# Optimization experiments

Hardware: AMD Instinct MI355X
Metric: run time of the kernel (lower is better)

Reference implementation:

```python
import jax, jax.numpy as jnp
import numpy as np

N = 50000      # nodes
E = 800000     # edges
D_IN = 128
D_H = 128
D_OUT = 64
P = 0.3        # dropout prob


def _glorot(key, out_c, in_c):
    return jax.random.normal(key, (out_c, in_c), jnp.float32) * (1.0 / np.sqrt(in_c))


def setup_inputs() -> dict:
    key = jax.random.key(0)
    ks = jax.random.split(key, 10)
    return {
        "x": jax.random.normal(ks[0], (N, D_IN), jnp.float32),
        "u1": jax.random.uniform(ks[1], (N, D_H), jnp.float32),
        "u2": jax.random.uniform(ks[2], (N, D_H), jnp.float32),
        "wl0": _glorot(ks[3], D_H, D_IN), "bl0": jnp.zeros((D_H,), jnp.float32), "wr0": _glorot(ks[4], D_H, D_IN),
        "wl1": _glorot(ks[5], D_H, D_H), "bl1": jnp.zeros((D_H,), jnp.float32), "wr1": _glorot(ks[6], D_H, D_H),
        "wl2": _glorot(ks[7], D_OUT, D_H), "bl2": jnp.zeros((D_OUT,), jnp.float32), "wr2": _glorot(ks[8], D_OUT, D_H),
        "edge_index": jax.random.randint(ks[9], (2, E), 0, N),
    }


def _sage_conv(x, src, dst, wl, bl, wr):
    # PyG SAGEConv (aggr='mean'): lin_l(mean of neighbor msgs) + lin_r(x)
    msg = x[src]                                                    # [E, d] gather
    s = jax.ops.segment_sum(msg, dst, num_segments=N)               # [N, d] scatter-sum
    cnt = jax.ops.segment_sum(jnp.ones((dst.shape[0],), x.dtype), dst, num_segments=N)
    mean = s / jnp.maximum(cnt, 1.0)[:, None]                       # mean; 0 for isolated nodes
    return mean @ wl.T + bl + x @ wr.T


def reference(x, u1, u2, wl0, bl0, wr0, wl1, bl1, wr1, wl2, bl2, wr2, edge_index):
    src, dst = edge_index[0], edge_index[1]
    keep = 1.0 - P
    h = jax.nn.relu(_sage_conv(x, src, dst, wl0, bl0, wr0))
    h = h * ((u1 >= P).astype(h.dtype) / keep)                      # dropout (training=True)
    h = jax.nn.relu(_sage_conv(h, src, dst, wl1, bl1, wr1))
    h = h * ((u2 >= P).astype(h.dtype) / keep)
    return _sage_conv(h, src, dst, wl2, bl2, wr2)
```

## Files before the change

### kernel.cpp

```cpp
#include <hip/hip_runtime.h>


constexpr int N = 50000;
constexpr int E = 800000;
constexpr int NBUCK = (N + 255) / 256;
constexpr int CE = 4096;
constexpr int NEB = (E + CE - 1) / CE;
constexpr int SLOT = 6208;
static_assert(N <= 65536, "u16 packing");
static_assert(N % 16 == 0, "16-row blocks need no bounds checks");

typedef _Float16 f16x8 __attribute__((ext_vector_type(8)));
typedef _Float16 f16x4 __attribute__((ext_vector_type(4)));
typedef _Float16 f16x2 __attribute__((ext_vector_type(2)));
typedef float f32x4 __attribute__((ext_vector_type(4)));
typedef unsigned short u16x8 __attribute__((ext_vector_type(8)));
typedef unsigned short u16x4 __attribute__((ext_vector_type(4)));

constexpr int CONVB = (N * 128 / 8 + 255) / 256;
constexpr int MASKB = (N * 128) / (8 * 256);

__device__ inline void wfrag_build(int idx, int KB, const float* wl,
                                   const float* wr, _Float16* wf) {
  int j = idx & 7;
  int lane = (idx >> 3) & 63;
  int kb = (idx >> 9) % KB;
  int ct = (idx >> 9) / KB;
  int c = ct * 16 + (lane & 15);
  int k = kb * 32 + (lane >> 4) * 8 + j;
  float v = (k < 128) ? wl[c * 128 + k] : wr[c * 128 + (k - 128)];
  wf[idx] = (_Float16)v;
}

__global__ __launch_bounds__(256) void setup_scatter_kernel(
    const int* __restrict__ src, const int* __restrict__ dst,
    int* __restrict__ bcur, unsigned* __restrict__ T,
    const float* __restrict__ x,
    const float* __restrict__ u1, const float* __restrict__ u2,
    const float* __restrict__ wl0, const float* __restrict__ wr0,
    const float* __restrict__ wl1, const float* __restrict__ wr1,
    const float* __restrict__ wl2, const float* __restrict__ wr2,
    _Float16* __restrict__ HA, _Float16* __restrict__ wf0,
    _Float16* __restrict__ wf1, _Float16* __restrict__ wfZ,
    unsigned* __restrict__ mk1, unsigned* __restrict__ mk2) {
  __shared__ unsigned sorted[CE];
  __shared__ int hist[256], scan[256], excl[256], lcur[256], gbase[256];
  const int b = blockIdx.x;
  const int t = threadIdx.x;
  if (b < NEB) {
    const int e0 = b * CE;
    const int nval = min(CE, E - e0);
    hist[t] = 0;
    __syncthreads();
    for (int i = t; i < nval; i += 256) atomicAdd(&hist[dst[e0 + i] >> 8], 1);
    __syncthreads();
    const int h = hist[t];
    scan[t] = h;
    __syncthreads();
    for (int off = 1; off < 256; off <<= 1) {
      int u = (t >= off) ? scan[t - off] : 0;
      __syncthreads();
      scan[t] += u;
      __syncthreads();
    }
    excl[t] = scan[t] - h;
    lcur[t] = scan[t] - h;
    gbase[t] = (t < NBUCK && h > 0) ? (t * SLOT + atomicAdd(&bcur[t], h)) : 0;
    __syncthreads();
    for (int i = t; i < nval; i += 256) {
      int e = e0 + i;
      int d = dst[e];
      int p = atomicAdd(&lcur[d >> 8], 1);
      sorted[p] = ((unsigned)d << 16) | (unsigned)src[e];
    }
    __syncthreads();
    for (int i = t; i < nval; i += 256) {
      unsigned pk = sorted[i];
      int bb = pk >> 24;
      T[gbase[bb] + (i - excl[bb])] = pk;
    }
    return;
  }
  const int b2 = b - NEB;
  if (b2 < CONVB) {
    int i = b2 * 256 + t;
    if (i < N * 128 / 8) {
      float4 a = ((const float4*)x)[i * 2];
      float4 c = ((const float4*)x)[i * 2 + 1];
      f16x8 v;
      v[0] = (_Float16)a.x; v[1] = (_Float16)a.y; v[2] = (_Float16)a.z; v[3] = (_Float16)a.w;
      v[4] = (_Float16)c.x; v[5] = (_Float16)c.y; v[6] = (_Float16)c.z; v[7] = (_Float16)c.w;
      ((f16x8*)HA)[i] = v;
    }
  } else if (b2 < CONVB + 128) {
    wfrag_build((b2 - CONVB) * 256 + t, 8, wl0, wr0, wf0);
  } else if (b2 < CONVB + 256) {
    wfrag_build((b2 - CONVB - 128) * 256 + t, 8, wl1, wr1, wf1);
  } else if (b2 < CONVB + 320) {
    int idx = (b2 - CONVB - 256) * 256 + t;
    int j = idx & 7;
    int lane = (idx >> 3) & 63;
    int kb = (idx >> 9) & 3;
    int ct = idx >> 11;
    int c = ct * 16 + (lane & 15);
    int k = kb * 32 + (lane >> 4) * 8 + j;
    float v = (c < 64) ? wl2[c * 128 + k] : wr2[(c - 64) * 128 + k];
    wfZ[idx] = (_Float16)v;
  } else {
    int mb = b2 - (CONVB + 320);
    const float* Us = (mb < MASKB) ? u1 : u2;
    unsigned* MKs = (mb < MASKB) ? mk1 : mk2;
    int bb = (mb < MASKB) ? mb : (mb - MASKB);
#pragma unroll
    for (int k = 0; k < 8; ++k) {
      int i = (bb * 8 + k) * 256 + t;
      unsigned long long m = __ballot(Us[i] >= 0.3f);
      int lt = t & 63;
      if (lt == 0) MKs[i >> 5] = (unsigned)m;
      else if (lt == 32) MKs[i >> 5] = (unsigned)(m >> 32);
    }
  }
}

__global__ __launch_bounds__(256) void bucket_place_kernel(
    const unsigned* __restrict__ T, const int* __restrict__ bcur,
    int* __restrict__ offs, int* __restrict__ deg,
    unsigned short* __restrict__ elist) {
  __shared__ int dcnt[256], s[256], ncur[256];
  const int t = threadIdx.x;
  const int b = blockIdx.x;
  const int lo = b * SLOT;
  const int hi = lo + bcur[b];
  dcnt[t] = 0;
  __syncthreads();
  for (int i = lo + t; i < hi; i += 256) atomicAdd(&dcnt[(T[i] >> 16) & 255], 1);
  __syncthreads();
  const int v = dcnt[t];
  const int pv = (v + 7) & ~7;
  s[t] = pv;
  __syncthreads();
  for (int off = 1; off < 256; off <<= 1) {
    int u = (t >= off) ? s[t - off] : 0;
    __syncthreads();
    s[t] += u;
    __syncthreads();
  }
  const int base = lo + s[t] - pv;
  const int node = b * 256 + t;
  if (node < N) { offs[node] = base; deg[node] = v; }
  ncur[t] = base;
  __syncthreads();
  for (int i = lo + t; i < hi; i += 256) {
    unsigned pk = T[i];
    int pos = atomicAdd(&ncur[(pk >> 16) & 255], 1);
    elist[pos] = (unsigned short)(pk & 0xffffu);
  }
}

__device__ __forceinline__ void gather_mean_wide(
    const _Float16* __restrict__ H, const unsigned short* __restrict__ elist,
    int e0, int d, int g, int cl, float* acc ) {
  const int e1 = e0 + d;
  int e = e0;
  for (; e + 16 <= e1; e += 16) {
    u16x8 q0 = *(const u16x8*)(elist + e);
    u16x8 q1 = *(const u16x8*)(elist + e + 8);
    int s[16] = {q0[0], q0[1], q0[2], q0[3], q0[4], q0[5], q0[6], q0[7],
                 q1[0], q1[1], q1[2], q1[3], q1[4], q1[5], q1[6], q1[7]};
    f16x8 v[8];
#pragma unroll
    for (int u = 0; u < 8; ++u)
      v[u] = *(const f16x8*)(H + (size_t)s[2 * u + g] * 128 + cl * 8);
#pragma unroll
    for (int u = 0; u < 8; ++u)
#pragma unroll
      for (int j = 0; j < 8; ++j) acc[j] += (float)v[u][j];
  }
  for (; e + 2 <= e1; e += 2) {
    int s0 = elist[e + g];
    f16x8 v = *(const f16x8*)(H + (size_t)s0 * 128 + cl * 8);
#pragma unroll
    for (int j = 0; j < 8; ++j) acc[j] += (float)v[j];
  }
  if (e < e1 && g == 0) {
    f16x8 v = *(const f16x8*)(H + (size_t)elist[e] * 128 + cl * 8);
#pragma unroll
    for (int j = 0; j < 8; ++j) acc[j] += (float)v[j];
  }
#pragma unroll
  for (int j = 0; j < 8; ++j) acc[j] += __shfl_xor(acc[j], 16);
}

__global__ __launch_bounds__(256, 6) void fused_layer_kernel(
    const _Float16* __restrict__ H, const int* __restrict__ offs,
    const int* __restrict__ deg, const unsigned short* __restrict__ elist,
    const _Float16* __restrict__ Wf, const float* __restrict__ bias,
    const unsigned* __restrict__ MK, _Float16* __restrict__ outp) {
  __shared__ __align__(16) _Float16 Af[8][64][8];
  const int t = threadIdx.x;
  const int rowbase = blockIdx.x * 16;

  {
    int r = t >> 4, o = t & 15;
    f16x8 v = *(const f16x8*)(H + (size_t)(rowbase + r) * 128 + o * 8);
    *(f16x8*)&Af[4 + (o >> 2)][(o & 3) * 16 + r][0] = v;
  }

  {
    const int hw = t >> 5;
    const int ll = t & 31;
    const int g = ll >> 4;
    const int cl = ll & 15;
#pragma unroll 1
    for (int i = 0; i < 2; ++i) {
      int r = hw * 2 + i;
      int node = rowbase + r;
      float acc[8] = {0.f, 0.f, 0.f, 0.f, 0.f, 0.f, 0.f, 0.f};
      const int d = deg[node];
      gather_mean_wide(H, elist, offs[node], d, g, cl, acc);
      if (g == 0) {
        float inv = 1.0f / (float)max(d, 1);
        f16x8 o;
#pragma unroll
        for (int j = 0; j < 8; ++j) o[j] = (_Float16)(acc[j] * inv);
        *(f16x8*)&Af[cl >> 2][(cl & 3) * 16 + r][0] = o;
      }
    }
  }
  __syncthreads();

  const int lane = t & 63;
  const int w = t >> 6;
  const int n16 = lane & 15;
  const int qq = lane >> 4;
  const int colbase = w * 32;

  f32x4 acc[2];
  acc[0] = (f32x4){0.f, 0.f, 0.f, 0.f};
  acc[1] = (f32x4){0.f, 0.f, 0.f, 0.f};

#pragma unroll
  for (int kb = 0; kb < 8; ++kb) {
    f16x8 a = *(const f16x8*)&Af[kb][lane][0];
#pragma unroll
    for (int ct = 0; ct < 2; ++ct) {
      const int ctg = w * 2 + ct;
      f16x8 b = *(const f16x8*)(Wf + ((size_t)(ctg * 8 + kb) * 64 + lane) * 8);
      acc[ct] = __builtin_amdgcn_mfma_f32_16x16x32_f16(a, b, acc[ct], 0, 0, 0);
    }
  }

#pragma unroll
  for (int r = 0; r < 4; ++r) {
    int row = rowbase + qq * 4 + r;
    unsigned mw = MK[(size_t)row * 4 + w];
#pragma unroll
    for (int ct = 0; ct < 2; ++ct) {
      const int col = colbase + ct * 16 + n16;
      float v = fmaxf(acc[ct][r] + bias[col], 0.f);
      v = ((mw >> (ct * 16 + n16)) & 1u) ? v * (1.0f / 0.7f) : 0.0f;
      outp[(size_t)row * 128 + col] = (_Float16)v;
    }
  }
}

__global__ __launch_bounds__(256, 6) void fused_layerZ_kernel(
    const _Float16* __restrict__ H, const int* __restrict__ offs,
    const int* __restrict__ deg, const unsigned short* __restrict__ elist,
    const _Float16* __restrict__ Wf, const float* __restrict__ bias,
    const unsigned* __restrict__ MK, const _Float16* __restrict__ WfZ,
    const float* __restrict__ bl2, _Float16* __restrict__ Y2,
    float* __restrict__ F) {
  __shared__ __align__(16) _Float16 Af[8][64][8];
  __shared__ __align__(16) _Float16 Zf[16][136];
  const int t = threadIdx.x;
  const int rowbase = blockIdx.x * 16;

  {
    int r = t >> 4, o = t & 15;
    f16x8 v = *(const f16x8*)(H + (size_t)(rowbase + r) * 128 + o * 8);
    *(f16x8*)&Af[4 + (o >> 2)][(o & 3) * 16 + r][0] = v;
  }

  {
    const int hw = t >> 5;
    const int ll = t & 31;
    const int g = ll >> 4;
    const int cl = ll & 15;
#pragma unroll 1
    for (int i = 0; i < 2; ++i) {
      int r = hw * 2 + i;
      int node = rowbase + r;
      float acc[8] = {0.f, 0.f, 0.f, 0.f, 0.f, 0.f, 0.f, 0.f};
      const int d = deg[node];
      gather_mean_wide(H, elist, offs[node], d, g, cl, acc);
      if (g == 0) {
        float inv = 1.0f / (float)max(d, 1);
        f16x8 o;
#pragma unroll
        for (int j = 0; j < 8; ++j) o[j] = (_Float16)(acc[j] * inv);
        *(f16x8*)&Af[cl >> 2][(cl & 3) * 16 + r][0] = o;
      }
    }
  }
  __syncthreads();

  const int lane = t & 63;
  const int w = t >> 6;
  const int n16 = lane & 15;
  const int qq = lane >> 4;
  const int colbase = w * 32;

  f32x4 acc[2];
  acc[0] = (f32x4){0.f, 0.f, 0.f, 0.f};
  acc[1] = (f32x4){0.f, 0.f, 0.f, 0.f};

#pragma unroll
  for (int kb = 0; kb < 8; ++kb) {
    f16x8 a = *(const f16x8*)&Af[kb][lane][0];
#pragma unroll
    for (int ct = 0; ct < 2; ++ct) {
      const int ctg = w * 2 + ct;
      f16x8 b = *(const f16x8*)(Wf + ((size_t)(ctg * 8 + kb) * 64 + lane) * 8);
      acc[ct] = __builtin_amdgcn_mfma_f32_16x16x32_f16(a, b, acc[ct], 0, 0, 0);
    }
  }

#pragma unroll
  for (int r = 0; r < 4; ++r) {
    int row = qq * 4 + r;
    unsigned mw = MK[(size_t)(rowbase + row) * 4 + w];
#pragma unroll
    for (int ct = 0; ct < 2; ++ct) {
      const int col = colbase + ct * 16 + n16;
      float v = fmaxf(acc[ct][r] + bias[col], 0.f);
      v = ((mw >> (ct * 16 + n16)) & 1u) ? v * (1.0f / 0.7f) : 0.0f;
      Zf[row][col] = (_Float16)v;
    }
  }
  __syncthreads();

  f32x4 az[2];
  az[0] = (f32x4){0.f, 0.f, 0.f, 0.f};
  az[1] = (f32x4){0.f, 0.f, 0.f, 0.f};
#pragma unroll
  for (int kb = 0; kb < 4; ++kb) {
    f16x8 a = *(const f16x8*)&Zf[n16][kb * 32 + qq * 8];
#pragma unroll
    for (int ct = 0; ct < 2; ++ct) {
      const int ctg = w * 2 + ct;
      f16x8 b = *(const f16x8*)(WfZ + ((size_t)(ctg * 4 + kb) * 64 + lane) * 8);
      az[ct] = __builtin_amdgcn_mfma_f32_16x16x32_f16(a, b, az[ct], 0, 0, 0);
    }
  }
#pragma unroll
  for (int ct = 0; ct < 2; ++ct) {
    const int col = colbase + ct * 16 + n16;
#pragma unroll
    for (int r = 0; r < 4; ++r) {
      int row = rowbase + qq * 4 + r;
      float v = az[ct][r];
      if (col < 64) Y2[(size_t)row * 64 + col] = (_Float16)v;
      else F[(size_t)row * 64 + (col - 64)] = v + bl2[col - 64];
    }
  }
}

__global__ __launch_bounds__(256, 8) void gather64_add_kernel(
    const _Float16* __restrict__ Y2, const float* __restrict__ F,
    const int* __restrict__ offs, const int* __restrict__ deg,
    const unsigned short* __restrict__ elist, float* __restrict__ out) {
  int node = blockIdx.x * 8 + (threadIdx.x >> 5);
  if (node >= N) return;
  const int ll = threadIdx.x & 31;
  const int g = ll >> 4;
  const int cl = ll & 15;
  const int e0 = offs[node];
  const int d = deg[node];
  const int e1 = e0 + d;
  float a0 = 0.f, a1 = 0.f, a2 = 0.f, a3 = 0.f;
  int e = e0;
  for (; e + 16 <= e1; e += 16) {
    u16x8 q0 = *(const u16x8*)(elist + e);
    u16x8 q1 = *(const u16x8*)(elist + e + 8);
    int s[16] = {q0[0], q0[1], q0[2], q0[3], q0[4], q0[5], q0[6], q0[7],
                 q1[0], q1[1], q1[2], q1[3], q1[4], q1[5], q1[6], q1[7]};
    f16x4 v[8];
#pragma unroll
    for (int u = 0; u < 8; ++u)
      v[u] = *(const f16x4*)(Y2 + (size_t)s[2 * u + g] * 64 + cl * 4);
#pragma unroll
    for (int u = 0; u < 8; ++u) {
      a0 += (float)v[u][0]; a1 += (float)v[u][1];
      a2 += (float)v[u][2]; a3 += (float)v[u][3];
    }
  }
  for (; e + 2 <= e1; e += 2) {
    int s0 = elist[e + g];
    f16x4 v = *(const f16x4*)(Y2 + (size_t)s0 * 64 + cl * 4);
    a0 += (float)v[0]; a1 += (float)v[1];
    a2 += (float)v[2]; a3 += (float)v[3];
  }
  if (e < e1 && g == 0) {
    f16x4 v = *(const f16x4*)(Y2 + (size_t)elist[e] * 64 + cl * 4);
    a0 += (float)v[0]; a1 += (float)v[1];
    a2 += (float)v[2]; a3 += (float)v[3];
  }
  a0 += __shfl_xor(a0, 16);
  a1 += __shfl_xor(a1, 16);
  a2 += __shfl_xor(a2, 16);
  a3 += __shfl_xor(a3, 16);
  if (g == 0) {
    float inv = 1.0f / (float)max(d, 1);
    float4 f = ((const float4*)(F + (size_t)node * 64))[cl];
    float4 o;
    o.x = f.x + a0 * inv;
    o.y = f.y + a1 * inv;
    o.z = f.z + a2 * inv;
    o.w = f.w + a3 * inv;
    ((float4*)(out + (size_t)node * 64))[cl] = o;
  }
}

extern "C" void kernel_launch(void* const* d_in, const int* in_sizes, int n_in,
                              void* d_out, int out_size, void* d_ws, size_t ws_size,
                              hipStream_t stream) {
  const float* x   = (const float*)d_in[0];
  const float* u1  = (const float*)d_in[1];
  const float* u2  = (const float*)d_in[2];
  const float* wl0 = (const float*)d_in[3];
  const float* bl0 = (const float*)d_in[4];
  const float* wr0 = (const float*)d_in[5];
  const float* wl1 = (const float*)d_in[6];
  const float* bl1 = (const float*)d_in[7];
  const float* wr1 = (const float*)d_in[8];
  const float* wl2 = (const float*)d_in[9];
  const float* bl2 = (const float*)d_in[10];
  const float* wr2 = (const float*)d_in[11];
  const int* edge  = (const int*)d_in[12];
  const int* src = edge;
  const int* dst = edge + E;

  _Float16* HA  = (_Float16*)d_ws;
  _Float16* HB  = HA + (size_t)N * 128;
  _Float16* Y2  = HB + (size_t)N * 128;
  float* F      = (float*)(Y2 + (size_t)N * 64);
  int* offs     = (int*)(F + (size_t)N * 64);
  int* deg      = offs + N;
  unsigned short* elist = (unsigned short*)(deg + N);
  unsigned* T   = (unsigned*)(elist + NBUCK * SLOT);
  int* bcur     = (int*)(T + NBUCK * SLOT);
  uintptr_t p = (uintptr_t)(bcur + NBUCK);
  p = (p + 15) & ~(uintptr_t)15;
  _Float16* wf0 = (_Float16*)p;
  _Float16* wf1 = wf0 + 8 * 8 * 512;
  _Float16* wfZ = wf1 + 8 * 8 * 512;
  unsigned* mk1 = (unsigned*)(wfZ + 8 * 4 * 512);
  unsigned* mk2 = mk1 + (size_t)N * 4;

  hipMemsetAsync(bcur, 0, NBUCK * sizeof(int), stream);
  setup_scatter_kernel<<<NEB + CONVB + 320 + 2 * MASKB, 256, 0, stream>>>(
      src, dst, bcur, T, x, u1, u2, wl0, wr0, wl1, wr1, wl2, wr2,
      HA, wf0, wf1, wfZ, mk1, mk2);
  bucket_place_kernel<<<NBUCK, 256, 0, stream>>>(T, bcur, offs, deg, elist);

  const int GM16 = N / 16;
  const int GG64 = (N + 7) / 8;

  fused_layer_kernel<<<GM16, 256, 0, stream>>>(HA, offs, deg, elist, wf0, bl0,
                                               mk1, HB);
  fused_layerZ_kernel<<<GM16, 256, 0, stream>>>(HB, offs, deg, elist, wf1, bl1,
                                                mk2, wfZ, bl2, Y2, F);
  gather64_add_kernel<<<GG64, 256, 0, stream>>>(Y2, F, offs, deg, elist,
                                                (float*)d_out);
}
```

Before: 290.6 us.

## Split feature matrices into 32-column slabs and unfuse gather from GEMM

Feature matrices are stored column-blocked, as four (or two) slabs of 32 half columns per node, so each gather kernel works on one slab at a time. The working set per pass is then smaller and more likely to stay in cache. Neighbor-mean aggregation moves out of the fused GEMM kernels into separate gather kernels that write an intermediate mean buffer, which reuses the scratch region of the edge sort. This trades extra kernel launches and an extra write and read of the mean matrix for better cache locality of the random gathers and higher occupancy.

```diff
diff --git a/kernel.cpp b/kernel.cpp
--- a/kernel.cpp
+++ b/kernel.cpp
@@ -7,15 +7,14 @@
 constexpr int CE = 4096;
 constexpr int NEB = (E + CE - 1) / CE;
 constexpr int SLOT = 6208;
+constexpr int GNB = (N + 63) / 64;
 static_assert(N <= 65536, "u16 packing");
-static_assert(N % 16 == 0, "16-row blocks need no bounds checks");
+static_assert(N % 16 == 0, "16-row gemm blocks need no bounds checks");
 
 typedef _Float16 f16x8 __attribute__((ext_vector_type(8)));
-typedef _Float16 f16x4 __attribute__((ext_vector_type(4)));
 typedef _Float16 f16x2 __attribute__((ext_vector_type(2)));
 typedef float f32x4 __attribute__((ext_vector_type(4)));
 typedef unsigned short u16x8 __attribute__((ext_vector_type(8)));
-typedef unsigned short u16x4 __attribute__((ext_vector_type(4)));
 
 constexpr int CONVB = (N * 128 / 8 + 255) / 256;
 constexpr int MASKB = (N * 128) / (8 * 256);
@@ -40,7 +39,7 @@
     const float* __restrict__ wl0, const float* __restrict__ wr0,
     const float* __restrict__ wl1, const float* __restrict__ wr1,
     const float* __restrict__ wl2, const float* __restrict__ wr2,
-    _Float16* __restrict__ HA, _Float16* __restrict__ wf0,
+    _Float16* __restrict__ HAcb, _Float16* __restrict__ wf0,
     _Float16* __restrict__ wf1, _Float16* __restrict__ wfZ,
     unsigned* __restrict__ mk1, unsigned* __restrict__ mk2) {
   __shared__ unsigned sorted[CE];
@@ -85,12 +84,13 @@
   if (b2 < CONVB) {
     int i = b2 * 256 + t;
     if (i < N * 128 / 8) {
+      int n = i >> 4, o = i & 15;
       float4 a = ((const float4*)x)[i * 2];
       float4 c = ((const float4*)x)[i * 2 + 1];
       f16x8 v;
       v[0] = (_Float16)a.x; v[1] = (_Float16)a.y; v[2] = (_Float16)a.z; v[3] = (_Float16)a.w;
       v[4] = (_Float16)c.x; v[5] = (_Float16)c.y; v[6] = (_Float16)c.z; v[7] = (_Float16)c.w;
-      ((f16x8*)HA)[i] = v;
+      *(f16x8*)(HAcb + ((size_t)(o >> 2) * N + n) * 32 + (o & 3) * 8) = v;
     }
   } else if (b2 < CONVB + 128) {
     wfrag_build((b2 - CONVB) * 256 + t, 8, wl0, wr0, wf0);
@@ -157,75 +157,68 @@
   }
 }
 
-__device__ __forceinline__ void gather_mean_wide(
-    const _Float16* __restrict__ H, const unsigned short* __restrict__ elist,
-    int e0, int d, int g, int cl, float* acc ) {
-  const int e1 = e0 + d;
-  int e = e0;
-  for (; e + 16 <= e1; e += 16) {
-    u16x8 q0 = *(const u16x8*)(elist + e);
-    u16x8 q1 = *(const u16x8*)(elist + e + 8);
-    int s[16] = {q0[0], q0[1], q0[2], q0[3], q0[4], q0[5], q0[6], q0[7],
-                 q1[0], q1[1], q1[2], q1[3], q1[4], q1[5], q1[6], q1[7]};
-    f16x8 v[8];
-#pragma unroll
-    for (int u = 0; u < 8; ++u)
-      v[u] = *(const f16x8*)(H + (size_t)s[2 * u + g] * 128 + cl * 8);
-#pragma unroll
-    for (int u = 0; u < 8; ++u)
-#pragma unroll
-      for (int j = 0; j < 8; ++j) acc[j] += (float)v[u][j];
-  }
-  for (; e + 2 <= e1; e += 2) {
-    int s0 = elist[e + g];
-    f16x8 v = *(const f16x8*)(H + (size_t)s0 * 128 + cl * 8);
-#pragma unroll
-    for (int j = 0; j < 8; ++j) acc[j] += (float)v[j];
-  }
-  if (e < e1 && g == 0) {
-    f16x8 v = *(const f16x8*)(H + (size_t)elist[e] * 128 + cl * 8);
-#pragma unroll
-    for (int j = 0; j < 8; ++j) acc[j] += (float)v[j];
-  }
-#pragma unroll
-  for (int j = 0; j < 8; ++j) acc[j] += __shfl_xor(acc[j], 16);
-}
-
-__global__ __launch_bounds__(256, 6) void fused_layer_kernel(
-    const _Float16* __restrict__ H, const int* __restrict__ offs,
+__global__ __launch_bounds__(256, 8) void gatherM_kernel(
+    const _Float16* __restrict__ Hcb, const int* __restrict__ offs,
     const int* __restrict__ deg, const unsigned short* __restrict__ elist,
+    _Float16* __restrict__ Mcb) {
+  const int s = blockIdx.x & 3;
+  const int nb = blockIdx.x >> 2;
+  const _Float16* Hs = Hcb + (size_t)s * N * 32;
+  _Float16* Ms = Mcb + (size_t)s * N * 32;
+  const int t = threadIdx.x;
+  const int hw = t >> 5;
+  const int ll = t & 31;
+  const int g = ll >> 4;
+  const int cl = ll & 15;
+#pragma unroll 1
+  for (int i = 0; i < 8; ++i) {
+    int node = nb * 64 + hw * 8 + i;
+    if (node >= N) break;
+    const int e0 = offs[node];
+    const int d = deg[node];
+    const int e1 = e0 + d;
+    float a0 = 0.f, a1 = 0.f;
+    int e = e0;
+    for (; e + 8 <= e1; e += 8) {
+      u16x8 qv = *(const u16x8*)(elist + e);
+      f16x2 v[4];
+#pragma unroll
+      for (int u = 0; u < 4; ++u)
+        v[u] = *(const f16x2*)(Hs + (size_t)qv[2 * u + g] * 32 + cl * 2);
+#pragma unroll
+      for (int u = 0; u < 4; ++u) { a0 += (float)v[u][0]; a1 += (float)v[u][1]; }
+    }
+    for (; e + 2 <= e1; e += 2) {
+      f16x2 v = *(const f16x2*)(Hs + (size_t)elist[e + g] * 32 + cl * 2);
+      a0 += (float)v[0]; a1 += (float)v[1];
+    }
+    if (e < e1 && g == 0) {
+      f16x2 v = *(const f16x2*)(Hs + (size_t)elist[e] * 32 + cl * 2);
+      a0 += (float)v[0]; a1 += (float)v[1];
+    }
+    a0 += __shfl_xor(a0, 16);
+    a1 += __shfl_xor(a1, 16);
+    if (g == 0) {
+      float inv = 1.0f / (float)max(d, 1);
+      f16x2 o;
+      o[0] = (_Float16)(a0 * inv); o[1] = (_Float16)(a1 * inv);
+      *(f16x2*)(Ms + (size_t)node * 32 + cl * 2) = o;
+    }
+  }
+}
+
+__global__ __launch_bounds__(256, 8) void gemm128_kernel(
+    const _Float16* __restrict__ Hcb, const _Float16* __restrict__ Mcb,
     const _Float16* __restrict__ Wf, const float* __restrict__ bias,
-    const unsigned* __restrict__ MK, _Float16* __restrict__ outp) {
+    const unsigned* __restrict__ MK, _Float16* __restrict__ outcb) {
   __shared__ __align__(16) _Float16 Af[8][64][8];
   const int t = threadIdx.x;
   const int rowbase = blockIdx.x * 16;
-
   {
     int r = t >> 4, o = t & 15;
-    f16x8 v = *(const f16x8*)(H + (size_t)(rowbase + r) * 128 + o * 8);
-    *(f16x8*)&Af[4 + (o >> 2)][(o & 3) * 16 + r][0] = v;
-  }
-
-  {
-    const int hw = t >> 5;
-    const int ll = t & 31;
-    const int g = ll >> 4;
-    const int cl = ll & 15;
-#pragma unroll 1
-    for (int i = 0; i < 2; ++i) {
-      int r = hw * 2 + i;
-      int node = rowbase + r;
-      float acc[8] = {0.f, 0.f, 0.f, 0.f, 0.f, 0.f, 0.f, 0.f};
-      const int d = deg[node];
-      gather_mean_wide(H, elist, offs[node], d, g, cl, acc);
-      if (g == 0) {
-        float inv = 1.0f / (float)max(d, 1);
-        f16x8 o;
-#pragma unroll
-        for (int j = 0; j < 8; ++j) o[j] = (_Float16)(acc[j] * inv);
-        *(f16x8*)&Af[cl >> 2][(cl & 3) * 16 + r][0] = o;
-      }
-    }
+    size_t base = ((size_t)(o >> 2) * N + rowbase + r) * 32 + (o & 3) * 8;
+    *(f16x8*)&Af[4 + (o >> 2)][(o & 3) * 16 + r][0] = *(const f16x8*)(Hcb + base);
+    *(f16x8*)&Af[o >> 2][(o & 3) * 16 + r][0] = *(const f16x8*)(Mcb + base);
   }
   __syncthreads();
 
@@ -238,7 +231,6 @@
   f32x4 acc[2];
   acc[0] = (f32x4){0.f, 0.f, 0.f, 0.f};
   acc[1] = (f32x4){0.f, 0.f, 0.f, 0.f};
-
 #pragma unroll
   for (int kb = 0; kb < 8; ++kb) {
     f16x8 a = *(const f16x8*)&Af[kb][lane][0];
@@ -249,7 +241,6 @@
       acc[ct] = __builtin_amdgcn_mfma_f32_16x16x32_f16(a, b, acc[ct], 0, 0, 0);
     }
   }
-
 #pragma unroll
   for (int r = 0; r < 4; ++r) {
     int row = rowbase + qq * 4 + r;
@@ -259,49 +250,26 @@
       const int col = colbase + ct * 16 + n16;
       float v = fmaxf(acc[ct][r] + bias[col], 0.f);
       v = ((mw >> (ct * 16 + n16)) & 1u) ? v * (1.0f / 0.7f) : 0.0f;
-      outp[(size_t)row * 128 + col] = (_Float16)v;
-    }
-  }
-}
-
-__global__ __launch_bounds__(256, 6) void fused_layerZ_kernel(
-    const _Float16* __restrict__ H, const int* __restrict__ offs,
-    const int* __restrict__ deg, const unsigned short* __restrict__ elist,
+      outcb[((size_t)(col >> 5) * N + row) * 32 + (col & 31)] = (_Float16)v;
+    }
+  }
+}
+
+__global__ __launch_bounds__(256, 8) void gemmZ_kernel(
+    const _Float16* __restrict__ Hcb, const _Float16* __restrict__ Mcb,
     const _Float16* __restrict__ Wf, const float* __restrict__ bias,
     const unsigned* __restrict__ MK, const _Float16* __restrict__ WfZ,
-    const float* __restrict__ bl2, _Float16* __restrict__ Y2,
+    const float* __restrict__ bl2, _Float16* __restrict__ Y2cb,
     float* __restrict__ F) {
   __shared__ __align__(16) _Float16 Af[8][64][8];
   __shared__ __align__(16) _Float16 Zf[16][136];
   const int t = threadIdx.x;
   const int rowbase = blockIdx.x * 16;
-
   {
     int r = t >> 4, o = t & 15;
-    f16x8 v = *(const f16x8*)(H + (size_t)(rowbase + r) * 128 + o * 8);
-    *(f16x8*)&Af[4 + (o >> 2)][(o & 3) * 16 + r][0] = v;
-  }
-
-  {
-    const int hw = t >> 5;
-    const int ll = t & 31;
-    const int g = ll >> 4;
-    const int cl = ll & 15;
-#pragma unroll 1
-    for (int i = 0; i < 2; ++i) {
-      int r = hw * 2 + i;
-      int node = rowbase + r;
-      float acc[8] = {0.f, 0.f, 0.f, 0.f, 0.f, 0.f, 0.f, 0.f};
-      const int d = deg[node];
-      gather_mean_wide(H, elist, offs[node], d, g, cl, acc);
-      if (g == 0) {
-        float inv = 1.0f / (float)max(d, 1);
-        f16x8 o;
-#pragma unroll
-        for (int j = 0; j < 8; ++j) o[j] = (_Float16)(acc[j] * inv);
-        *(f16x8*)&Af[cl >> 2][(cl & 3) * 16 + r][0] = o;
-      }
-    }
+    size_t base = ((size_t)(o >> 2) * N + rowbase + r) * 32 + (o & 3) * 8;
+    *(f16x8*)&Af[4 + (o >> 2)][(o & 3) * 16 + r][0] = *(const f16x8*)(Hcb + base);
+    *(f16x8*)&Af[o >> 2][(o & 3) * 16 + r][0] = *(const f16x8*)(Mcb + base);
   }
   __syncthreads();
 
@@ -314,7 +282,6 @@
   f32x4 acc[2];
   acc[0] = (f32x4){0.f, 0.f, 0.f, 0.f};
   acc[1] = (f32x4){0.f, 0.f, 0.f, 0.f};
-
 #pragma unroll
   for (int kb = 0; kb < 8; ++kb) {
     f16x8 a = *(const f16x8*)&Af[kb][lane][0];
@@ -325,7 +292,6 @@
       acc[ct] = __builtin_amdgcn_mfma_f32_16x16x32_f16(a, b, acc[ct], 0, 0, 0);
     }
   }
-
 #pragma unroll
   for (int r = 0; r < 4; ++r) {
     int row = qq * 4 + r;
@@ -360,65 +326,63 @@
     for (int r = 0; r < 4; ++r) {
       int row = rowbase + qq * 4 + r;
       float v = az[ct][r];
-      if (col < 64) Y2[(size_t)row * 64 + col] = (_Float16)v;
-      else F[(size_t)row * 64 + (col - 64)] = v + bl2[col - 64];
-    }
-  }
-}
-
-__global__ __launch_bounds__(256, 8) void gather64_add_kernel(
-    const _Float16* __restrict__ Y2, const float* __restrict__ F,
+      if (col < 64)
+        Y2cb[((size_t)(col >> 5) * N + row) * 32 + (col & 31)] = (_Float16)v;
+      else
+        F[(size_t)row * 64 + (col - 64)] = v + bl2[col - 64];
+    }
+  }
+}
+
+__global__ __launch_bounds__(256, 8) void gatherY_kernel(
+    const _Float16* __restrict__ Y2cb, const float* __restrict__ F,
     const int* __restrict__ offs, const int* __restrict__ deg,
     const unsigned short* __restrict__ elist, float* __restrict__ out) {
-  int node = blockIdx.x * 8 + (threadIdx.x >> 5);
-  if (node >= N) return;
-  const int ll = threadIdx.x & 31;
+  const int s = blockIdx.x & 1;
+  const int nb = blockIdx.x >> 1;
+  const _Float16* Ys = Y2cb + (size_t)s * N * 32;
+  const int t = threadIdx.x;
+  const int hw = t >> 5;
+  const int ll = t & 31;
   const int g = ll >> 4;
   const int cl = ll & 15;
-  const int e0 = offs[node];
-  const int d = deg[node];
-  const int e1 = e0 + d;
-  float a0 = 0.f, a1 = 0.f, a2 = 0.f, a3 = 0.f;
-  int e = e0;
-  for (; e + 16 <= e1; e += 16) {
-    u16x8 q0 = *(const u16x8*)(elist + e);
-    u16x8 q1 = *(const u16x8*)(elist + e + 8);
-    int s[16] = {q0[0], q0[1], q0[2], q0[3], q0[4], q0[5], q0[6], q0[7],
-                 q1[0], q1[1], q1[2], q1[3], q1[4], q1[5], q1[6], q1[7]};
-    f16x4 v[8];
-#pragma unroll
-    for (int u = 0; u < 8; ++u)
-      v[u] = *(const f16x4*)(Y2 + (size_t)s[2 * u + g] * 64 + cl * 4);
-#pragma unroll
-    for (int u = 0; u < 8; ++u) {
-      a0 += (float)v[u][0]; a1 += (float)v[u][1];
-      a2 += (float)v[u][2]; a3 += (float)v[u][3];
-    }
-  }
-  for (; e + 2 <= e1; e += 2) {
-    int s0 = elist[e + g];
-    f16x4 v = *(const f16x4*)(Y2 + (size_t)s0 * 64 + cl * 4);
-    a0 += (float)v[0]; a1 += (float)v[1];
-    a2 += (float)v[2]; a3 += (float)v[3];
-  }
-  if (e < e1 && g == 0) {
-    f16x4 v = *(const f16x4*)(Y2 + (size_t)elist[e] * 64 + cl * 4);
-    a0 += (float)v[0]; a1 += (float)v[1];
-    a2 += (float)v[2]; a3 += (float)v[3];
-  }
-  a0 += __shfl_xor(a0, 16);
-  a1 += __shfl_xor(a1, 16);
-  a2 += __shfl_xor(a2, 16);
-  a3 += __shfl_xor(a3, 16);
-  if (g == 0) {
-    float inv = 1.0f / (float)max(d, 1);
-    float4 f = ((const float4*)(F + (size_t)node * 64))[cl];
-    float4 o;
-    o.x = f.x + a0 * inv;
-    o.y = f.y + a1 * inv;
-    o.z = f.z + a2 * inv;
-    o.w = f.w + a3 * inv;
-    ((float4*)(out + (size_t)node * 64))[cl] = o;
+#pragma unroll 1
+  for (int i = 0; i < 8; ++i) {
+    int node = nb * 64 + hw * 8 + i;
+    if (node >= N) break;
+    const int e0 = offs[node];
+    const int d = deg[node];
+    const int e1 = e0 + d;
+    float a0 = 0.f, a1 = 0.f;
+    int e = e0;
+    for (; e + 8 <= e1; e += 8) {
+      u16x8 qv = *(const u16x8*)(elist + e);
+      f16x2 v[4];
+#pragma unroll
+      for (int u = 0; u < 4; ++u)
+        v[u] = *(const f16x2*)(Ys + (size_t)qv[2 * u + g] * 32 + cl * 2);
+#pragma unroll
+      for (int u = 0; u < 4; ++u) { a0 += (float)v[u][0]; a1 += (float)v[u][1]; }
+    }
+    for (; e + 2 <= e1; e += 2) {
+      f16x2 v = *(const f16x2*)(Ys + (size_t)elist[e + g] * 32 + cl * 2);
+      a0 += (float)v[0]; a1 += (float)v[1];
+    }
+    if (e < e1 && g == 0) {
+      f16x2 v = *(const f16x2*)(Ys + (size_t)elist[e] * 32 + cl * 2);
+      a0 += (float)v[0]; a1 += (float)v[1];
+    }
+    a0 += __shfl_xor(a0, 16);
+    a1 += __shfl_xor(a1, 16);
+    if (g == 0) {
+      float inv = 1.0f / (float)max(d, 1);
+      const float* fp = F + (size_t)node * 64 + s * 32 + cl * 2;
+      float2 f = *(const float2*)fp;
+      float2 o;
+      o.x = f.x + a0 * inv;
+      o.y = f.y + a1 * inv;
+      *(float2*)(out + (size_t)node * 64 + s * 32 + cl * 2) = o;
+    }
   }
 }
 
@@ -441,15 +405,19 @@
   const int* src = edge;
   const int* dst = edge + E;
 
-  _Float16* HA  = (_Float16*)d_ws;
-  _Float16* HB  = HA + (size_t)N * 128;
-  _Float16* Y2  = HB + (size_t)N * 128;
-  float* F      = (float*)(Y2 + (size_t)N * 64);
+  _Float16* HAcb = (_Float16*)d_ws;
+  _Float16* HBcb = HAcb + (size_t)N * 128;
+  _Float16* Y2cb = HBcb + (size_t)N * 128;
+  float* F      = (float*)(Y2cb + (size_t)N * 64);
   int* offs     = (int*)(F + (size_t)N * 64);
   int* deg      = offs + N;
   unsigned short* elist = (unsigned short*)(deg + N);
-  unsigned* T   = (unsigned*)(elist + NBUCK * SLOT);
-  int* bcur     = (int*)(T + NBUCK * SLOT);
+  uintptr_t pu = (uintptr_t)(elist + NBUCK * SLOT);
+  pu = (pu + 15) & ~(uintptr_t)15;
+  unsigned* T   = (unsigned*)pu;
+  _Float16* Mcb = (_Float16*)pu;
+  uintptr_t p2 = pu + (size_t)N * 128 * sizeof(_Float16);
+  int* bcur     = (int*)p2;
   uintptr_t p = (uintptr_t)(bcur + NBUCK);
   p = (p + 15) & ~(uintptr_t)15;
   _Float16* wf0 = (_Float16*)p;
@@ -461,16 +429,14 @@
   hipMemsetAsync(bcur, 0, NBUCK * sizeof(int), stream);
   setup_scatter_kernel<<<NEB + CONVB + 320 + 2 * MASKB, 256, 0, stream>>>(
       src, dst, bcur, T, x, u1, u2, wl0, wr0, wl1, wr1, wl2, wr2,
-      HA, wf0, wf1, wfZ, mk1, mk2);
+      HAcb, wf0, wf1, wfZ, mk1, mk2);
   bucket_place_kernel<<<NBUCK, 256, 0, stream>>>(T, bcur, offs, deg, elist);
 
-  const int GM16 = N / 16;
-  const int GG64 = (N + 7) / 8;
-
-  fused_layer_kernel<<<GM16, 256, 0, stream>>>(HA, offs, deg, elist, wf0, bl0,
-                                               mk1, HB);
-  fused_layerZ_kernel<<<GM16, 256, 0, stream>>>(HB, offs, deg, elist, wf1, bl1,
-                                                mk2, wfZ, bl2, Y2, F);
-  gather64_add_kernel<<<GG64, 256, 0, stream>>>(Y2, F, offs, deg, elist,
-                                                (float*)d_out);
-}
+  gatherM_kernel<<<4 * GNB, 256, 0, stream>>>(HAcb, offs, deg, elist, Mcb);
+  gemm128_kernel<<<N / 16, 256, 0, stream>>>(HAcb, Mcb, wf0, bl0, mk1, HBcb);
+  gatherM_kernel<<<4 * GNB, 256, 0, stream>>>(HBcb, offs, deg, elist, Mcb);
+  gemmZ_kernel<<<N / 16, 256, 0, stream>>>(HBcb, Mcb, wf1, bl1, mk2, wfZ, bl2,
+                                           Y2cb, F);
+  gatherY_kernel<<<2 * GNB, 256, 0, stream>>>(Y2cb, F, offs, deg, elist,
+                                              (float*)d_out);
+}
```

Result: slower. 357.7 us (+23.1%).
